# Kernel optimization log

Hardware: AMD Instinct MI355X
Metric: run time of the kernel (lower is better)

The kernel has to match this reference:

```python
import jax, jax.numpy as jnp
import numpy as np

BS, N, K, S = 512, 500, 100, 96  # batch, nodes per sample, kriged nodes per sample, seq_len
HID, AUG = 32, 2
TAU = 0.1


def setup_inputs() -> dict:
    key = jax.random.key(0)
    ks = jax.random.split(key, 8)
    x = jax.random.normal(ks[0], (BS * N, S), jnp.float32)
    y = jax.random.normal(ks[1], (BS * N, S), jnp.float32)
    W1 = jax.random.normal(ks[2], (S, HID), jnp.float32) / np.sqrt(S)
    b1 = jnp.zeros((HID,), jnp.float32)
    W2 = jax.random.normal(ks[3], (HID, AUG), jnp.float32) / np.sqrt(HID)
    b2 = jnp.zeros((AUG,), jnp.float32)
    # unique node indices per sample (torch index-assign with dups is ill-defined)
    perm_keys = jax.random.split(ks[4], BS)
    krig_idx = jax.vmap(lambda k: jax.random.permutation(k, N)[:K])(perm_keys).astype(jnp.int32)
    idx_of_node = jnp.full((BS,), N, jnp.int32)  # nodes per sample
    mask = (jax.random.uniform(ks[5], (BS * K, S)) > 0.1).astype(jnp.float32)
    gumbel = jax.random.gumbel(ks[6], (BS * K, AUG), jnp.float32)
    return {"x": x, "y": y, "W1": W1, "b1": b1, "W2": W2, "b2": b2,
            "mask": mask, "gumbel": gumbel, "krig_idx": krig_idx,
            "idx_of_node": idx_of_node}


def reference(x, y, W1, b1, W2, b2, mask, gumbel, krig_idx, idx_of_node):
    bs, k = krig_idx.shape
    num_nodes = x.shape[0] // bs
    s = x.shape[1]
    # gather kriged node series: [bs, num_nodes, S] -> [bs*K, S]
    y3 = y.reshape(bs, num_nodes, s)
    smp = jnp.take_along_axis(y3, krig_idx[:, :, None], axis=1).reshape(bs * k, s)
    # tiny MLP on gathered features (krig_feat == smp, same gather done twice in torch)
    h = jax.nn.relu(smp @ W1 + b1)
    logits = h @ W2 + b2
    # hard gumbel-softmax, straight-through
    y_soft = jax.nn.softmax((logits + gumbel) / TAU, axis=-1)
    y_hard = jax.nn.one_hot(jnp.argmax(y_soft, axis=-1), logits.shape[-1], dtype=y_soft.dtype)
    gb = y_hard - jax.lax.stop_gradient(y_soft) + y_soft  # [bs*K, 2]
    # data_aug = [zeros, mask*smp] (detached); sum over aug dim == gb[:,1]*masked
    val = gb[:, 1:2] * jax.lax.stop_gradient(mask * smp)  # [bs*K, S]
    # flat row indices: per-sample offsets from shifted cumsum of idx_of_node
    offs = jnp.cumsum(jnp.concatenate([jnp.zeros((1,), idx_of_node.dtype), idx_of_node])[:-1])
    flat = (offs[:, None] + krig_idx).reshape(-1)  # [bs*K]
    return x.at[flat].set(val)
```

## Files before the change

### kernel.cpp

```cpp
#include <hip/hip_runtime.h>

#define BSZ 512
#define NN  500
#define KK  100
#define SS  96
#define HIDN 32
#define ROWS (BSZ * NN)
#define NF4  (ROWS * SS / 4)
#define F4PR (SS / 4)
#define NSLOT 12
#define FUSE_BLOCKS 2048
#define FUSE_STRIDE (FUSE_BLOCKS * 256)

typedef float vf4 __attribute__((ext_vector_type(4)));

__global__ __launch_bounds__(512) void prep_kernel(const int* __restrict__ idx_of_node,
                                                   int* __restrict__ offs,
                                                   int* __restrict__ flag) {
    if (blockIdx.x == 0) {
        __shared__ int buf[BSZ];
        int t = threadIdx.x;
        int v = idx_of_node[t];
        buf[t] = v;
        __syncthreads();
        int acc = v;
        for (int d = 1; d < BSZ; d <<= 1) {
            int add = (t >= d) ? buf[t - d] : 0;
            __syncthreads();
            acc += add;
            buf[t] = acc;
            __syncthreads();
        }
        offs[t] = acc - v;
    }
    int4* f4 = reinterpret_cast<int4*>(flag);
    int n4 = ROWS / 4;
    for (int i = blockIdx.x * 512 + threadIdx.x; i < n4; i += gridDim.x * 512)
        f4[i] = make_int4(-1, -1, -1, -1);
}

__global__ __launch_bounds__(256) void gate_kernel(
    const float* __restrict__ y, const float* __restrict__ W1,
    const float* __restrict__ b1, const float* __restrict__ W2,
    const float* __restrict__ b2, const float* __restrict__ gumbel,
    const int* __restrict__ krig_idx, const int* __restrict__ offs,
    int* __restrict__ flag, float* __restrict__ gate) {
    __shared__ float4 w1s[SS * HIDN / 4];
    __shared__ float b1s[HIDN];
    __shared__ float w2s[HIDN * 2];
    __shared__ float b2s[2];
    for (int i = threadIdx.x; i < SS * HIDN / 4; i += 256)
        w1s[i] = reinterpret_cast<const float4*>(W1)[i];
    if (threadIdx.x < HIDN) b1s[threadIdx.x] = b1[threadIdx.x];
    if (threadIdx.x < 2 * HIDN) w2s[threadIdx.x] = W2[threadIdx.x];
    if (threadIdx.x < 2) b2s[threadIdx.x] = b2[threadIdx.x];
    __syncthreads();

    int r = blockIdx.x * 256 + threadIdx.x;
    if (r >= BSZ * KK) return;
    int b = r / KK;
    int node = krig_idx[r];
    const float4* yrow = reinterpret_cast<const float4*>(y + (size_t)(b * NN + node) * SS);

    float h[HIDN];
#pragma unroll
    for (int j = 0; j < HIDN; ++j) h[j] = b1s[j];
#pragma unroll
    for (int s4 = 0; s4 < F4PR; ++s4) {
        float4 v = yrow[s4];
        float vv[4] = {v.x, v.y, v.z, v.w};
        const float4* wbase = &w1s[s4 * 4 * (HIDN / 4)];
#pragma unroll
        for (int q = 0; q < 4; ++q) {
#pragma unroll
            for (int j4 = 0; j4 < HIDN / 4; ++j4) {
                float4 w = wbase[q * (HIDN / 4) + j4];
                h[j4 * 4 + 0] += vv[q] * w.x;
                h[j4 * 4 + 1] += vv[q] * w.y;
                h[j4 * 4 + 2] += vv[q] * w.z;
                h[j4 * 4 + 3] += vv[q] * w.w;
            }
        }
    }
    float l0 = b2s[0], l1 = b2s[1];
#pragma unroll
    for (int j = 0; j < HIDN; ++j) {
        float hr = fmaxf(h[j], 0.0f);
        l0 += hr * w2s[j * 2 + 0];
        l1 += hr * w2s[j * 2 + 1];
    }
    float g0 = gumbel[r * 2 + 0], g1 = gumbel[r * 2 + 1];
    gate[r] = (l1 + g1 > l0 + g0) ? 1.0f : 0.0f;
    flag[offs[b] + node] = r;
}

__global__ __launch_bounds__(256) void fuse_kernel(
    const vf4* __restrict__ x4, const vf4* __restrict__ y4,
    const vf4* __restrict__ mask4, const float* __restrict__ gate,
    const int* __restrict__ flag, const int* __restrict__ krig_idx,
    vf4* __restrict__ out4) {
    const int t = blockIdx.x * 256 + threadIdx.x;

    vf4 xv[NSLOT];
    int fr[NSLOT];
#pragma unroll
    for (int k = 0; k < NSLOT; ++k) {
        int idx = t + k * FUSE_STRIDE;
        if (idx < NF4) {
            xv[k] = x4[idx];
            fr[k] = flag[idx / F4PR];
        } else {
            fr[k] = -1;
        }
    }
#pragma unroll
    for (int k = 0; k < NSLOT; ++k) {
        int r = fr[k];
        if (r >= 0) {
            int idx = t + k * FUSE_STRIDE;
            int row = idx / F4PR;
            int c = idx - row * F4PR;
            int b = r / KK;
            int node = krig_idx[r];
            float g = gate[r];
            vf4 m = mask4[r * F4PR + c];
            vf4 v = y4[(b * NN + node) * F4PR + c];
            xv[k] = g * m * v;
        }
    }
#pragma unroll
    for (int k = 0; k < NSLOT; ++k) {
        int idx = t + k * FUSE_STRIDE;
        if (idx < NF4) __builtin_nontemporal_store(xv[k], out4 + idx);
    }
}

extern "C" void kernel_launch(void* const* d_in, const int* in_sizes, int n_in,
                              void* d_out, int out_size, void* d_ws, size_t ws_size,
                              hipStream_t stream) {
    const float* x      = (const float*)d_in[0];
    const float* y      = (const float*)d_in[1];
    const float* W1     = (const float*)d_in[2];
    const float* b1     = (const float*)d_in[3];
    const float* W2     = (const float*)d_in[4];
    const float* b2     = (const float*)d_in[5];
    const float* mask   = (const float*)d_in[6];
    const float* gumbel = (const float*)d_in[7];
    const int* krig_idx = (const int*)d_in[8];
    const int* idx_of_node = (const int*)d_in[9];
    float* out = (float*)d_out;

    int* offs = (int*)d_ws;
    int* flag = offs + BSZ;
    float* gate = (float*)(flag + ROWS);

    prep_kernel<<<128, 512, 0, stream>>>(idx_of_node, offs, flag);

    int rows = BSZ * KK;
    gate_kernel<<<(rows + 255) / 256, 256, 0, stream>>>(
        y, W1, b1, W2, b2, gumbel, krig_idx, offs, flag, gate);

    fuse_kernel<<<FUSE_BLOCKS, 256, 0, stream>>>(
        reinterpret_cast<const vf4*>(x), reinterpret_cast<const vf4*>(y),
        reinterpret_cast<const vf4*>(mask), gate, flag, krig_idx,
        reinterpret_cast<vf4*>(out));
}
```

Before: 68.30 us.

## Pack gather source row and gate into per-row int2 flag; skip x reads for kriged rows

The gate kernel now writes a packed int2 per output row holding the source y-row index (or -2 when the gate is off) and the kriged row id. The separate gate array and the krig_idx lookup in the fuse pass go away. The fuse kernel reads x only for untouched rows, writes zeros without any loads for gated-off rows, and loads mask and y only for gated-on rows. The fuse pass also switches from a grid-stride layout to a contiguous per-block tile of 8 slots with an exact grid. In exchange the flag buffer doubles in size, which adds init and read traffic in the prep and fuse passes.

New measurement: 59.53 us. 12.8% less time.

```diff
diff --git a/kernel.cpp b/kernel.cpp
--- a/kernel.cpp
+++ b/kernel.cpp
@@ -8,15 +8,15 @@
 #define ROWS (BSZ * NN)
 #define NF4  (ROWS * SS / 4)
 #define F4PR (SS / 4)
-#define NSLOT 12
-#define FUSE_BLOCKS 2048
-#define FUSE_STRIDE (FUSE_BLOCKS * 256)
+#define NSLOT 8
+#define FUSE_BLOCKS (NF4 / (256 * NSLOT))
 
 typedef float vf4 __attribute__((ext_vector_type(4)));
 
+
 __global__ __launch_bounds__(512) void prep_kernel(const int* __restrict__ idx_of_node,
                                                    int* __restrict__ offs,
-                                                   int* __restrict__ flag) {
+                                                   int4* __restrict__ flag2_4) {
     if (blockIdx.x == 0) {
         __shared__ int buf[BSZ];
         int t = threadIdx.x;
@@ -33,10 +33,9 @@
         }
         offs[t] = acc - v;
     }
-    int4* f4 = reinterpret_cast<int4*>(flag);
-    int n4 = ROWS / 4;
+    int n4 = ROWS / 2;
     for (int i = blockIdx.x * 512 + threadIdx.x; i < n4; i += gridDim.x * 512)
-        f4[i] = make_int4(-1, -1, -1, -1);
+        flag2_4[i] = make_int4(-1, 0, -1, 0);
 }
 
 __global__ __launch_bounds__(256) void gate_kernel(
@@ -44,7 +43,7 @@
     const float* __restrict__ b1, const float* __restrict__ W2,
     const float* __restrict__ b2, const float* __restrict__ gumbel,
     const int* __restrict__ krig_idx, const int* __restrict__ offs,
-    int* __restrict__ flag, float* __restrict__ gate) {
+    int2* __restrict__ flag2) {
     __shared__ float4 w1s[SS * HIDN / 4];
     __shared__ float b1s[HIDN];
     __shared__ float w2s[HIDN * 2];
@@ -90,48 +89,42 @@
         l1 += hr * w2s[j * 2 + 1];
     }
     float g0 = gumbel[r * 2 + 0], g1 = gumbel[r * 2 + 1];
-    gate[r] = (l1 + g1 > l0 + g0) ? 1.0f : 0.0f;
-    flag[offs[b] + node] = r;
+    int on = (l1 + g1 > l0 + g0);
+    flag2[offs[b] + node] = make_int2(on ? (b * NN + node) : -2, r);
 }
 
 __global__ __launch_bounds__(256) void fuse_kernel(
     const vf4* __restrict__ x4, const vf4* __restrict__ y4,
-    const vf4* __restrict__ mask4, const float* __restrict__ gate,
-    const int* __restrict__ flag, const int* __restrict__ krig_idx,
+    const vf4* __restrict__ mask4, const int2* __restrict__ flag2,
     vf4* __restrict__ out4) {
-    const int t = blockIdx.x * 256 + threadIdx.x;
+    const int t0 = blockIdx.x * (256 * NSLOT) + threadIdx.x;
 
-    vf4 xv[NSLOT];
-    int fr[NSLOT];
+    int2 fg[NSLOT];
 #pragma unroll
     for (int k = 0; k < NSLOT; ++k) {
-        int idx = t + k * FUSE_STRIDE;
-        if (idx < NF4) {
-            xv[k] = x4[idx];
-            fr[k] = flag[idx / F4PR];
-        } else {
-            fr[k] = -1;
+        int idx = t0 + k * 256;
+        fg[k] = flag2[idx / F4PR];
+    }
+    vf4 xv[NSLOT];
+#pragma unroll
+    for (int k = 0; k < NSLOT; ++k) {
+        int idx = t0 + k * 256;
+        int code = fg[k].x;
+        vf4 v = (vf4)(0.0f);
+        if (code == -1) {
+            v = x4[idx];
+        } else if (code >= 0) {
+            int row = idx / F4PR;
+            int c = idx - row * F4PR;
+            vf4 m = mask4[fg[k].y * F4PR + c];
+            v = m * y4[code * F4PR + c];
         }
+        xv[k] = v;
     }
 #pragma unroll
     for (int k = 0; k < NSLOT; ++k) {
-        int r = fr[k];
-        if (r >= 0) {
-            int idx = t + k * FUSE_STRIDE;
-            int row = idx / F4PR;
-            int c = idx - row * F4PR;
-            int b = r / KK;
-            int node = krig_idx[r];
-            float g = gate[r];
-            vf4 m = mask4[r * F4PR + c];
-            vf4 v = y4[(b * NN + node) * F4PR + c];
-            xv[k] = g * m * v;
-        }
-    }
-#pragma unroll
-    for (int k = 0; k < NSLOT; ++k) {
-        int idx = t + k * FUSE_STRIDE;
-        if (idx < NF4) __builtin_nontemporal_store(xv[k], out4 + idx);
+        int idx = t0 + k * 256;
+        __builtin_nontemporal_store(xv[k], out4 + idx);
     }
 }
 
@@ -151,17 +144,17 @@
     float* out = (float*)d_out;
 
     int* offs = (int*)d_ws;
-    int* flag = offs + BSZ;
-    float* gate = (float*)(flag + ROWS);
+    int2* flag2 = (int2*)(offs + BSZ);
 
-    prep_kernel<<<128, 512, 0, stream>>>(idx_of_node, offs, flag);
+    prep_kernel<<<128, 512, 0, stream>>>(idx_of_node, offs,
+                                         reinterpret_cast<int4*>(flag2));
 
     int rows = BSZ * KK;
     gate_kernel<<<(rows + 255) / 256, 256, 0, stream>>>(
-        y, W1, b1, W2, b2, gumbel, krig_idx, offs, flag, gate);
+        y, W1, b1, W2, b2, gumbel, krig_idx, offs, flag2);
 
     fuse_kernel<<<FUSE_BLOCKS, 256, 0, stream>>>(
         reinterpret_cast<const vf4*>(x), reinterpret_cast<const vf4*>(y),
-        reinterpret_cast<const vf4*>(mask), gate, flag, krig_idx,
+        reinterpret_cast<const vf4*>(mask), flag2,
         reinterpret_cast<vf4*>(out));
 }
```
